# Performance work log

Measured on AMD Instinct MI355X. Metric: run time of the kernel, lower is better.

## Reference

```python
import jax, jax.numpy as jnp
import numpy as np

TWO_PI = 2.0 * np.pi
OMEGA = 1.0  # frequency scale from init


def setup_inputs() -> dict:
    key = jax.random.key(0)
    ks = jax.random.split(key, 10)
    B, G, D = 2, 32, 3
    C_IN, C, C_OUT, F, L = 4, 128, 2, 128, 4  # in/model/out channels, freqs, n_spectral_convs
    a = jax.random.normal(ks[0], (B, G, G, G, C_IN), dtype=jnp.float32)
    x = jax.random.uniform(ks[1], (B, G, G, G, D), dtype=jnp.float32)
    y = jax.random.uniform(ks[2], (B, G, G, G, D), dtype=jnp.float32)
    fc_in_w = jax.random.normal(ks[3], (C_IN, C), dtype=jnp.float32) / np.sqrt(C_IN)
    fc_in_b = jnp.zeros((C,), dtype=jnp.float32)
    freqs = jax.random.normal(ks[4], (L, F, D), dtype=jnp.float32)  # per-layer spatial frequencies
    w_real = jax.random.normal(ks[5], (L, C, C, F), dtype=jnp.float32) * 0.05
    w_imag = jax.random.normal(ks[6], (L, C, C, F), dtype=jnp.float32) * 0.05
    fc_out_w = jax.random.normal(ks[7], (C, C_OUT), dtype=jnp.float32) / np.sqrt(C)
    fc_out_b = jnp.zeros((C_OUT,), dtype=jnp.float32)
    return {"a": a, "x": x, "y": y, "fc_in_w": fc_in_w, "fc_in_b": fc_in_b,
            "freqs": freqs, "w_real": w_real, "w_imag": w_imag,
            "fc_out_w": fc_out_w, "fc_out_b": fc_out_b}


def _spectral_conv(hf, xin, xout, k, Wc):
    # hf: (B, N, C) real; xin/xout: (B, N, D); k: (F, D); Wc: (C, C, F) complex
    N = hf.shape[1]
    ang_in = TWO_PI * OMEGA * jnp.einsum('bnd,fd->bnf', xin, k)
    phi_in = jnp.exp(-1j * ang_in.astype(jnp.complex64))          # (B, N, F)
    H = jnp.einsum('bnc,bnf->bcf', hf.astype(jnp.complex64), phi_in) / N  # forward transform
    G = jnp.einsum('bcf,cof->bof', H, Wc)                          # per-frequency channel mixing
    ang_out = TWO_PI * OMEGA * jnp.einsum('bnd,fd->bnf', xout, k)
    phi_out = jnp.exp(1j * ang_out.astype(jnp.complex64))          # (B, N, F)
    return jnp.real(jnp.einsum('bof,bnf->bno', G, phi_out))       # inverse evaluation at xout


def reference(a, x, y, fc_in_w, fc_in_b, freqs, w_real, w_imag, fc_out_w, fc_out_b):
    B = a.shape[0]
    spatial = a.shape[1:4]
    hf = jnp.einsum('...i,io->...o', a, fc_in_w) + fc_in_b
    hf = hf.reshape(B, -1, hf.shape[-1])               # (B, N, C)
    xf = x.reshape(B, -1, x.shape[-1])                 # (B, N, D)
    yf = y.reshape(B, -1, y.shape[-1])
    L = freqs.shape[0]
    for l in range(L):
        Wc = (w_real[l] + 1j * w_imag[l]).astype(jnp.complex64)
        pts_out = xf if l < L - 1 else yf              # last conv queries at y
        hf = jax.nn.gelu(_spectral_conv(hf, xf, pts_out, freqs[l], Wc))
    u = jnp.einsum('bnc,co->bno', hf, fc_out_w) + fc_out_b
    return u.reshape(B, *spatial, fc_out_w.shape[-1])
```

## Files before the change

kernel.cpp:

```cpp
#include <hip/hip_runtime.h>
#include <math.h>

#define Bb 2
#define Nn 32768
#define Cc 128
#define Ff 128
#define LL 4
#define SKN 128
#define PS 16448

typedef __attribute__((ext_vector_type(8))) short short8;
typedef __attribute__((ext_vector_type(4))) float float4v;
typedef __attribute__((ext_vector_type(2))) unsigned int uint2v;
typedef unsigned short ushort_t;
typedef unsigned int uint_t;

union frag_cast { short8 s; uint_t u[4]; };
union vec8 { float4v v[2]; float s[8]; };

__device__ inline uint_t asu(float f) { union { float f; uint_t u; } x; x.f = f; return x.u; }
__device__ inline float asf(uint_t u) { union { uint_t u; float f; } x; x.u = u; return x.f; }
__device__ inline uint_t pack_hi(float v0, float v1) {
    return __builtin_amdgcn_perm(asu(v1), asu(v0), 0x07060302u);
}
__device__ inline float resid(float v) { return v - asf(asu(v) & 0xffff0000u); }

typedef __attribute__((address_space(1))) const uint_t guint;
typedef __attribute__((address_space(3))) uint_t luint;
__device__ inline void gload16(const uint_t* g, uint_t* l) {
    __builtin_amdgcn_global_load_lds((guint*)g, (luint*)l, 16, 0, 0);
}

__global__ __launch_bounds__(256) void prep_xt(const float* __restrict__ x,
                                               const float* __restrict__ y,
                                               float* __restrict__ xT,
                                               float* __restrict__ yT) {
    int i = blockIdx.x * 256 + threadIdx.x;
    int b = i >> 15, n = i & 32767;
    const float* xp = x + (size_t)i * 3;
    const float* yp = y + (size_t)i * 3;
    size_t base = ((size_t)(b * 3) << 15) + n;
    xT[base] = xp[0]; xT[base + (1 << 15)] = xp[1]; xT[base + (2 << 15)] = xp[2];
    yT[base] = yp[0]; yT[base + (1 << 15)] = yp[1]; yT[base + (2 << 15)] = yp[2];
}

__global__ __launch_bounds__(256) void in_proj(const float* __restrict__ a,
                                               const float* __restrict__ w,
                                               const float* __restrict__ bias,
                                               uint_t* __restrict__ hfTh,
                                               uint_t* __restrict__ hfTl) {
    int idx = blockIdx.x * 256 + threadIdx.x;
    int np = idx & 16383;
    int c = (idx >> 14) & 127;
    int b = idx >> 21;
    int n = np * 2;
    const float* ap = a + (((size_t)(b << 15)) + n) * 4;
    float s0 = bias[c], s1 = s0;
#pragma unroll
    for (int i = 0; i < 4; ++i) { s0 += ap[i] * w[i * Cc + c]; s1 += ap[4 + i] * w[i * Cc + c]; }
    hfTh[idx] = pack_hi(s0, s1);
    hfTl[idx] = pack_hi(resid(s0), resid(s1));
}

__global__ __launch_bounds__(256) void fwd_lds(const uint_t* __restrict__ hfTh,
                                               const uint_t* __restrict__ hfTl,
                                               const float* __restrict__ xT,
                                               const float* __restrict__ freqs,
                                               float* __restrict__ Spart) {
    __shared__ __align__(16) uint_t Ah_s[2][1024], Al_s[2][1024];

    const int sk = blockIdx.x;
    const int ct = blockIdx.y & 1, ft = blockIdx.y >> 1;
    const int b = blockIdx.z;
    const int tid = threadIdx.x, lane = tid & 63, wave = tid >> 6;
    const int h = wave & 1, wn = wave >> 1;
    const int fr = lane & 15, kg = lane >> 4;
    const int crow0 = b * 128 + ct * 64;

    float kx[2], ky[2], kz[2];
#pragma unroll
    for (int ni = 0; ni < 2; ++ni) {
        int f = ft * 64 + wn * 32 + ni * 16 + fr;
        kx[ni] = freqs[f * 3 + 0];
        ky[ni] = freqs[f * 3 + 1];
        kz[ni] = freqs[f * 3 + 2];
    }

    const float* xb = xT + ((size_t)(b * 3) << 15);

    const int srow = wave * 16 + (lane >> 2);
    const size_t gbase = ((size_t)(crow0 + srow) << 14) + (size_t)((lane & 3) * 4);
    const int npair0 = sk * 128;

    float4v acc[4][2];
#pragma unroll
    for (int mi = 0; mi < 4; ++mi)
#pragma unroll
        for (int ni = 0; ni < 2; ++ni) acc[mi][ni] = (float4v){0.f, 0.f, 0.f, 0.f};

    vec8 X0[2], X1[2], X2[2];
    gload16(hfTh + gbase + npair0, &Ah_s[0][wave * 256]);
    gload16(hfTl + gbase + npair0, &Al_s[0][wave * 256]);
    {
        const int nbase = sk * 256 + kg * 8;
        X0[0].v[0] = *(const float4v*)(xb + nbase);
        X0[0].v[1] = *(const float4v*)(xb + nbase + 4);
        X1[0].v[0] = *(const float4v*)(xb + (1 << 15) + nbase);
        X1[0].v[1] = *(const float4v*)(xb + (1 << 15) + nbase + 4);
        X2[0].v[0] = *(const float4v*)(xb + (2 << 15) + nbase);
        X2[0].v[1] = *(const float4v*)(xb + (2 << 15) + nbase + 4);
    }

#pragma unroll
    for (int kt = 0; kt < 8; ++kt) {
        const int cur = kt & 1, nxt = cur ^ 1;
        __syncthreads();
        if (kt < 7) {
            gload16(hfTh + gbase + npair0 + (kt + 1) * 16, &Ah_s[nxt][wave * 256]);
            gload16(hfTl + gbase + npair0 + (kt + 1) * 16, &Al_s[nxt][wave * 256]);
            const int nbase2 = sk * 256 + (kt + 1) * 32 + kg * 8;
            X0[nxt].v[0] = *(const float4v*)(xb + nbase2);
            X0[nxt].v[1] = *(const float4v*)(xb + nbase2 + 4);
            X1[nxt].v[0] = *(const float4v*)(xb + (1 << 15) + nbase2);
            X1[nxt].v[1] = *(const float4v*)(xb + (1 << 15) + nbase2 + 4);
            X2[nxt].v[0] = *(const float4v*)(xb + (2 << 15) + nbase2);
            X2[nxt].v[1] = *(const float4v*)(xb + (2 << 15) + nbase2 + 4);
        }
        float r[16], tv[16];
#pragma unroll
        for (int ni = 0; ni < 2; ++ni)
#pragma unroll
            for (int q = 0; q < 4; ++q) {
                float rv0 = X0[cur].s[2 * q] * kx[ni] + X1[cur].s[2 * q] * ky[ni] + X2[cur].s[2 * q] * kz[ni];
                float rv1 = X0[cur].s[2 * q + 1] * kx[ni] + X1[cur].s[2 * q + 1] * ky[ni] + X2[cur].s[2 * q + 1] * kz[ni];
                r[ni * 8 + 2 * q] = __builtin_amdgcn_fractf(rv0);
                r[ni * 8 + 2 * q + 1] = __builtin_amdgcn_fractf(rv1);
            }
        if (h) {
#pragma unroll
            for (int i = 0; i < 16; ++i) tv[i] = __builtin_amdgcn_sinf(r[i]);
        } else {
#pragma unroll
            for (int i = 0; i < 16; ++i) tv[i] = __builtin_amdgcn_cosf(r[i]);
        }
        frag_cast bh[2], bl[2];
#pragma unroll
        for (int ni = 0; ni < 2; ++ni)
#pragma unroll
            for (int q = 0; q < 4; ++q) {
                float v0 = tv[ni * 8 + 2 * q], v1 = tv[ni * 8 + 2 * q + 1];
                bh[ni].u[q] = pack_hi(v0, v1);
                bl[ni].u[q] = pack_hi(resid(v0), resid(v1));
            }
#pragma unroll
        for (int mi = 0; mi < 4; ++mi) {
            frag_cast ah, al;
            ah.s = *(const short8*)&Ah_s[cur][(mi * 16 + fr) * 16 + kg * 4];
            al.s = *(const short8*)&Al_s[cur][(mi * 16 + fr) * 16 + kg * 4];
#pragma unroll
            for (int ni = 0; ni < 2; ++ni) {
                acc[mi][ni] = __builtin_amdgcn_mfma_f32_16x16x32_bf16(ah.s, bh[ni].s, acc[mi][ni], 0, 0, 0);
                acc[mi][ni] = __builtin_amdgcn_mfma_f32_16x16x32_bf16(ah.s, bl[ni].s, acc[mi][ni], 0, 0, 0);
                acc[mi][ni] = __builtin_amdgcn_mfma_f32_16x16x32_bf16(al.s, bh[ni].s, acc[mi][ni], 0, 0, 0);
            }
        }
    }

    float* op = Spart + (size_t)((b * 2 + h) * SKN + sk) * PS;
#pragma unroll
    for (int mi = 0; mi < 4; ++mi)
#pragma unroll
        for (int ni = 0; ni < 2; ++ni)
#pragma unroll
            for (int r2 = 0; r2 < 4; ++r2) {
                int c = ct * 64 + mi * 16 + kg * 4 + r2;
                int f = ft * 64 + wn * 32 + ni * 16 + fr;
                op[c * 128 + f] = acc[mi][ni][r2];
            }
}

__global__ __launch_bounds__(256) void reduce_kernel(const float* __restrict__ Spart,
                                                     float* __restrict__ S) {
    __shared__ float red[4][64];
    const int chunk = blockIdx.x, bh = blockIdx.y;
    const int tid = threadIdx.x;
    const int cfl = tid & 63, q = tid >> 6;
    const float* p = Spart + (size_t)bh * SKN * PS + (size_t)(q * 32) * PS + chunk * 64 + cfl;
    float s = 0.0f;
#pragma unroll 8
    for (int k = 0; k < 32; ++k) s += p[(size_t)k * PS];
    red[q][cfl] = s;
    __syncthreads();
    if (tid < 64) {
        float t = red[0][tid] + red[1][tid] + red[2][tid] + red[3][tid];
        S[bh * 16384 + chunk * 64 + tid] = t;
    }
}

__global__ __launch_bounds__(256) void mix_kernel(const float* __restrict__ S,
                                                  const float* __restrict__ Wre,
                                                  const float* __restrict__ Wim,
                                                  uint_t* __restrict__ Gh,
                                                  uint_t* __restrict__ Gl) {
    __shared__ float Stile[4][128][16];
    const int ot = blockIdx.x;
    const int ft = blockIdx.y;
    const int tid = threadIdx.x;
    const int fl = tid & 15, ol = (tid >> 4) & 1, cg = tid >> 5;
    const int o = ot * 2 + ol, f0 = ft * 16;

    for (int i = tid; i < 8192; i += 256) {
        int bh = i >> 11, c = (i >> 4) & 127, ff = i & 15;
        Stile[bh][c][ff] = S[(size_t)bh * 16384 + c * 128 + f0 + ff];
    }
    __syncthreads();

    float g0 = 0.f, g1 = 0.f, g2 = 0.f, g3 = 0.f;
#pragma unroll 4
    for (int c = cg * 16; c < cg * 16 + 16; ++c) {
        float wr = Wre[((size_t)(c * 128 + o)) * 128 + f0 + fl];
        float wi = Wim[((size_t)(c * 128 + o)) * 128 + f0 + fl];
        float sc0 = Stile[0][c][fl], ss0 = Stile[1][c][fl];
        float sc1 = Stile[2][c][fl], ss1 = Stile[3][c][fl];
        g0 += sc0 * wr + ss0 * wi;  g1 += ss0 * wr - sc0 * wi;
        g2 += sc1 * wr + ss1 * wi;  g3 += ss1 * wr - sc1 * wi;
    }
    __syncthreads();
    float4v* rp = (float4v*)Stile;
    rp[cg * 32 + ol * 16 + fl] = (float4v){g0, g1, g2, g3};
    __syncthreads();
    if (tid < 32) {
        int tol = tid >> 4, tfl = tid & 15;
        float4v r = rp[tid];
#pragma unroll
        for (int j = 1; j < 8; ++j) r += rp[j * 32 + tid];
        const float invN = 1.0f / (float)Nn;
        float gre0 = r[0] * invN, gmi0 = r[1] * invN;
        float gre1 = r[2] * invN, gmi1 = r[3] * invN;
        int oo = ot * 2 + tol;
        Gh[(0 * 128 + oo) * 128 + f0 + tfl] = pack_hi(gre0, gmi0);
        Gl[(0 * 128 + oo) * 128 + f0 + tfl] = pack_hi(resid(gre0), resid(gmi0));
        Gh[(1 * 128 + oo) * 128 + f0 + tfl] = pack_hi(gre1, gmi1);
        Gl[(1 * 128 + oo) * 128 + f0 + tfl] = pack_hi(resid(gre1), resid(gmi1));
    }
}

__global__ __launch_bounds__(256, 2) void inv_reg(const uint_t* __restrict__ Gh,
                                                  const uint_t* __restrict__ Gl,
                                                  const float* __restrict__ ptsT,
                                                  const float* __restrict__ freqs,
                                                  uint_t* __restrict__ hfTh,
                                                  uint_t* __restrict__ hfTl) {
    __shared__ __align__(16) float kxs[128], kys[128], kzs[128];
    const int nt = blockIdx.x, b = blockIdx.y;
    const int tid = threadIdx.x, lane = tid & 63, wn = tid >> 6;
    const int fr = lane & 15, kg = lane >> 4;

    if (tid < 128) {
        kxs[tid] = freqs[tid * 3 + 0];
        kys[tid] = freqs[tid * 3 + 1];
        kzs[tid] = freqs[tid * 3 + 2];
    }
    __syncthreads();

    frag_cast bh[8][2], bl[8][2];
#pragma unroll
    for (int kt = 0; kt < 8; ++kt)
#pragma unroll
        for (int ni = 0; ni < 2; ++ni) {
            size_t gi = ((size_t)(b * 128 + wn * 32 + ni * 16 + fr)) * 128 + kt * 16 + kg * 4;
            bh[kt][ni].s = *(const short8*)(Gh + gi);
            bl[kt][ni].s = *(const short8*)(Gl + gi);
        }

    const float* pb = ptsT + ((size_t)(b * 3) << 15);
    const int stripe0 = nt * 128;

    for (int it = 0; it < 4; ++it) {
        const int n0 = stripe0 + it * 32;
        float px[2], py[2], pz[2];
#pragma unroll
        for (int mi = 0; mi < 2; ++mi) {
            int n = n0 + mi * 16 + fr;
            px[mi] = pb[n]; py[mi] = pb[(1 << 15) + n]; pz[mi] = pb[(2 << 15) + n];
        }
        float4v acc[2][2];
#pragma unroll
        for (int mi = 0; mi < 2; ++mi)
#pragma unroll
            for (int ni = 0; ni < 2; ++ni) acc[mi][ni] = (float4v){0.f, 0.f, 0.f, 0.f};

#pragma unroll
        for (int kt = 0; kt < 8; ++kt) {
            float4v kxv = *(const float4v*)&kxs[kt * 16 + kg * 4];
            float4v kyv = *(const float4v*)&kys[kt * 16 + kg * 4];
            float4v kzv = *(const float4v*)&kzs[kt * 16 + kg * 4];
#pragma unroll
            for (int mi = 0; mi < 2; ++mi) {
                frag_cast ah, al;
#pragma unroll
                for (int q = 0; q < 4; ++q) {
                    float rev = px[mi] * kxv[q] + py[mi] * kyv[q] + pz[mi] * kzv[q];
                    float rr = __builtin_amdgcn_fractf(rev);
                    float cv = __builtin_amdgcn_cosf(rr);
                    float sv = __builtin_amdgcn_sinf(rr);
                    ah.u[q] = pack_hi(cv, sv);
                    al.u[q] = pack_hi(resid(cv), resid(sv));
                }
#pragma unroll
                for (int ni = 0; ni < 2; ++ni) {
                    acc[mi][ni] = __builtin_amdgcn_mfma_f32_16x16x32_bf16(ah.s, bh[kt][ni].s, acc[mi][ni], 0, 0, 0);
                    acc[mi][ni] = __builtin_amdgcn_mfma_f32_16x16x32_bf16(ah.s, bl[kt][ni].s, acc[mi][ni], 0, 0, 0);
                    acc[mi][ni] = __builtin_amdgcn_mfma_f32_16x16x32_bf16(al.s, bh[kt][ni].s, acc[mi][ni], 0, 0, 0);
                }
            }
        }

#pragma unroll
        for (int mi = 0; mi < 2; ++mi)
#pragma unroll
            for (int ni = 0; ni < 2; ++ni) {
                float g[4];
#pragma unroll
                for (int r2 = 0; r2 < 4; ++r2) {
                    float v = acc[mi][ni][r2];
                    float u2 = 1.5957691216057308f * (v + 0.044715f * v * v * v);
                    float t = 1.0f - 2.0f / (1.0f + __expf(u2));
                    g[r2] = 0.5f * v * (1.0f + t);
                }
                int o = wn * 32 + ni * 16 + fr;
                int nb = n0 + mi * 16 + kg * 4;
                size_t di = ((size_t)(b * 128 + o) << 14) + (nb >> 1);
                uint2v hv = { pack_hi(g[0], g[1]), pack_hi(g[2], g[3]) };
                uint2v lv = { pack_hi(resid(g[0]), resid(g[1])), pack_hi(resid(g[2]), resid(g[3])) };
                *(uint2v*)(hfTh + di) = hv;
                *(uint2v*)(hfTl + di) = lv;
            }
    }
}

__global__ __launch_bounds__(256) void out_proj(const uint_t* __restrict__ hfTh,
                                                const uint_t* __restrict__ hfTl,
                                                const float* __restrict__ w,
                                                const float* __restrict__ bias,
                                                float* __restrict__ u) {
    int i = blockIdx.x * 256 + threadIdx.x;
    int b = i >> 14, np = i & 16383;
    const uint_t* hp = hfTh + ((size_t)(b * 128) << 14) + np;
    const uint_t* lp = hfTl + ((size_t)(b * 128) << 14) + np;
    float s0a = bias[0], s1a = bias[1], s0b = bias[0], s1b = bias[1];
#pragma unroll 4
    for (int c = 0; c < 128; ++c) {
        uint_t hv = hp[(size_t)c << 14], lv = lp[(size_t)c << 14];
        float v0 = asf(hv << 16) + asf(lv << 16);
        float v1 = asf(hv & 0xffff0000u) + asf(lv & 0xffff0000u);
        float w0 = w[c * 2 + 0], w1 = w[c * 2 + 1];
        s0a += v0 * w0; s1a += v0 * w1;
        s0b += v1 * w0; s1b += v1 * w1;
    }
    float4v o4 = {s0a, s1a, s0b, s1b};
    *(float4v*)(u + ((size_t)(b << 15) + np * 2) * 2) = o4;
}

extern "C" void kernel_launch(void* const* d_in, const int* in_sizes, int n_in,
                              void* d_out, int out_size, void* d_ws, size_t ws_size,
                              hipStream_t stream) {
    const float* a        = (const float*)d_in[0];
    const float* x        = (const float*)d_in[1];
    const float* y        = (const float*)d_in[2];
    const float* fc_in_w  = (const float*)d_in[3];
    const float* fc_in_b  = (const float*)d_in[4];
    const float* freqs    = (const float*)d_in[5];
    const float* w_real   = (const float*)d_in[6];
    const float* w_imag   = (const float*)d_in[7];
    const float* fc_out_w = (const float*)d_in[8];
    const float* fc_out_b = (const float*)d_in[9];
    float* out = (float*)d_out;

    uint_t* ws    = (uint_t*)d_ws;
    uint_t* hfTh  = ws;
    uint_t* hfTl  = hfTh + (size_t)Bb * Cc * Nn / 2;
    float*  Spart = (float*)(hfTl + (size_t)Bb * Cc * Nn / 2);
    float*  S     = Spart + (size_t)Bb * 2 * SKN * PS;
    uint_t* Gh    = (uint_t*)(S + (size_t)Bb * 2 * Cc * Ff);
    uint_t* Gl    = Gh + (size_t)Bb * Cc * Ff;
    float*  xT    = (float*)(Gl + (size_t)Bb * Cc * Ff);
    float*  yT    = xT + (size_t)Bb * 3 * Nn;

    prep_xt<<<(Bb * Nn) / 256, 256, 0, stream>>>(x, y, xT, yT);
    in_proj<<<(Bb * Cc * Nn / 2) / 256, 256, 0, stream>>>(a, fc_in_w, fc_in_b, hfTh, hfTl);

    for (int l = 0; l < LL; ++l) {
        const float* k   = freqs  + (size_t)l * Ff * 3;
        const float* Wre = w_real + (size_t)l * Cc * Cc * Ff;
        const float* Wim = w_imag + (size_t)l * Cc * Cc * Ff;
        const float* pT  = (l < LL - 1) ? xT : yT;

        fwd_lds<<<dim3(SKN, 4, Bb), 256, 0, stream>>>(hfTh, hfTl, xT, k, Spart);
        reduce_kernel<<<dim3(256, 4), 256, 0, stream>>>(Spart, S);
        mix_kernel<<<dim3(64, 8), 256, 0, stream>>>(S, Wre, Wim, Gh, Gl);
        inv_reg<<<dim3(256, Bb), 256, 0, stream>>>(Gh, Gl, pT, k, hfTh, hfTl);
    }

    out_proj<<<(Bb * Nn / 2) / 256, 256, 0, stream>>>(hfTh, hfTl, fc_out_w, fc_out_b, out);
}
```

Baseline: 402.3 us.

## Share inverse phase fragments via LDS and split output channels across blocks

The inverse kernel changes its work split. Each block now handles 32 points and half of the output channels, launched on a (1024,2,B) grid. Each wave computes the cos/sin fragments for only two of the eight frequency tiles and shares them through LDS, instead of every wave recomputing all of them. This cuts redundant transcendental work and register pressure, allowing 4 blocks per CU, but adds LDS barriers, doubles phase computation across the two channel-half blocks, and drops the per-block loop over four stripes. The forward kernel now stages the point coordinates into LDS with one async global-to-LDS load instead of per-iteration register loads, and also raises its occupancy hint to 4.

```diff
diff --git a/kernel.cpp b/kernel.cpp
--- a/kernel.cpp
+++ b/kernel.cpp
@@ -30,6 +30,8 @@
 __device__ inline void gload16(const uint_t* g, uint_t* l) {
     __builtin_amdgcn_global_load_lds((guint*)g, (luint*)l, 16, 0, 0);
 }
+
+#define LBAR() asm volatile("s_waitcnt lgkmcnt(0)\n\ts_barrier" ::: "memory")
 
 __global__ __launch_bounds__(256) void prep_xt(const float* __restrict__ x,
                                                const float* __restrict__ y,
@@ -62,12 +64,13 @@
     hfTl[idx] = pack_hi(resid(s0), resid(s1));
 }
 
-__global__ __launch_bounds__(256) void fwd_lds(const uint_t* __restrict__ hfTh,
-                                               const uint_t* __restrict__ hfTl,
-                                               const float* __restrict__ xT,
-                                               const float* __restrict__ freqs,
-                                               float* __restrict__ Spart) {
+__global__ __launch_bounds__(256, 4) void fwd_lds(const uint_t* __restrict__ hfTh,
+                                                  const uint_t* __restrict__ hfTl,
+                                                  const float* __restrict__ xT,
+                                                  const float* __restrict__ freqs,
+                                                  float* __restrict__ Spart) {
     __shared__ __align__(16) uint_t Ah_s[2][1024], Al_s[2][1024];
+    __shared__ __align__(16) float Xs[768];
 
     const int sk = blockIdx.x;
     const int ct = blockIdx.y & 1, ft = blockIdx.y >> 1;
@@ -98,18 +101,12 @@
 #pragma unroll
         for (int ni = 0; ni < 2; ++ni) acc[mi][ni] = (float4v){0.f, 0.f, 0.f, 0.f};
 
-    vec8 X0[2], X1[2], X2[2];
+    if (wave < 3) {
+        const uint_t* gx = (const uint_t*)xb + ((size_t)wave << 15) + sk * 256 + lane * 4;
+        gload16(gx, (uint_t*)&Xs[wave * 256]);
+    }
     gload16(hfTh + gbase + npair0, &Ah_s[0][wave * 256]);
     gload16(hfTl + gbase + npair0, &Al_s[0][wave * 256]);
-    {
-        const int nbase = sk * 256 + kg * 8;
-        X0[0].v[0] = *(const float4v*)(xb + nbase);
-        X0[0].v[1] = *(const float4v*)(xb + nbase + 4);
-        X1[0].v[0] = *(const float4v*)(xb + (1 << 15) + nbase);
-        X1[0].v[1] = *(const float4v*)(xb + (1 << 15) + nbase + 4);
-        X2[0].v[0] = *(const float4v*)(xb + (2 << 15) + nbase);
-        X2[0].v[1] = *(const float4v*)(xb + (2 << 15) + nbase + 4);
-    }
 
 #pragma unroll
     for (int kt = 0; kt < 8; ++kt) {
@@ -118,21 +115,21 @@
         if (kt < 7) {
             gload16(hfTh + gbase + npair0 + (kt + 1) * 16, &Ah_s[nxt][wave * 256]);
             gload16(hfTl + gbase + npair0 + (kt + 1) * 16, &Al_s[nxt][wave * 256]);
-            const int nbase2 = sk * 256 + (kt + 1) * 32 + kg * 8;
-            X0[nxt].v[0] = *(const float4v*)(xb + nbase2);
-            X0[nxt].v[1] = *(const float4v*)(xb + nbase2 + 4);
-            X1[nxt].v[0] = *(const float4v*)(xb + (1 << 15) + nbase2);
-            X1[nxt].v[1] = *(const float4v*)(xb + (1 << 15) + nbase2 + 4);
-            X2[nxt].v[0] = *(const float4v*)(xb + (2 << 15) + nbase2);
-            X2[nxt].v[1] = *(const float4v*)(xb + (2 << 15) + nbase2 + 4);
-        }
+        }
+        vec8 x0, x1, x2;
+        x0.v[0] = *(const float4v*)&Xs[0 * 256 + kt * 32 + kg * 8];
+        x0.v[1] = *(const float4v*)&Xs[0 * 256 + kt * 32 + kg * 8 + 4];
+        x1.v[0] = *(const float4v*)&Xs[1 * 256 + kt * 32 + kg * 8];
+        x1.v[1] = *(const float4v*)&Xs[1 * 256 + kt * 32 + kg * 8 + 4];
+        x2.v[0] = *(const float4v*)&Xs[2 * 256 + kt * 32 + kg * 8];
+        x2.v[1] = *(const float4v*)&Xs[2 * 256 + kt * 32 + kg * 8 + 4];
         float r[16], tv[16];
 #pragma unroll
         for (int ni = 0; ni < 2; ++ni)
 #pragma unroll
             for (int q = 0; q < 4; ++q) {
-                float rv0 = X0[cur].s[2 * q] * kx[ni] + X1[cur].s[2 * q] * ky[ni] + X2[cur].s[2 * q] * kz[ni];
-                float rv1 = X0[cur].s[2 * q + 1] * kx[ni] + X1[cur].s[2 * q + 1] * ky[ni] + X2[cur].s[2 * q + 1] * kz[ni];
+                float rv0 = x0.s[2 * q] * kx[ni] + x1.s[2 * q] * ky[ni] + x2.s[2 * q] * kz[ni];
+                float rv1 = x0.s[2 * q + 1] * kx[ni] + x1.s[2 * q + 1] * ky[ni] + x2.s[2 * q + 1] * kz[ni];
                 r[ni * 8 + 2 * q] = __builtin_amdgcn_fractf(rv0);
                 r[ni * 8 + 2 * q + 1] = __builtin_amdgcn_fractf(rv1);
             }
@@ -143,14 +140,14 @@
 #pragma unroll
             for (int i = 0; i < 16; ++i) tv[i] = __builtin_amdgcn_cosf(r[i]);
         }
-        frag_cast bh[2], bl[2];
+        frag_cast bhf[2], blf[2];
 #pragma unroll
         for (int ni = 0; ni < 2; ++ni)
 #pragma unroll
             for (int q = 0; q < 4; ++q) {
                 float v0 = tv[ni * 8 + 2 * q], v1 = tv[ni * 8 + 2 * q + 1];
-                bh[ni].u[q] = pack_hi(v0, v1);
-                bl[ni].u[q] = pack_hi(resid(v0), resid(v1));
+                bhf[ni].u[q] = pack_hi(v0, v1);
+                blf[ni].u[q] = pack_hi(resid(v0), resid(v1));
             }
 #pragma unroll
         for (int mi = 0; mi < 4; ++mi) {
@@ -159,9 +156,9 @@
             al.s = *(const short8*)&Al_s[cur][(mi * 16 + fr) * 16 + kg * 4];
 #pragma unroll
             for (int ni = 0; ni < 2; ++ni) {
-                acc[mi][ni] = __builtin_amdgcn_mfma_f32_16x16x32_bf16(ah.s, bh[ni].s, acc[mi][ni], 0, 0, 0);
-                acc[mi][ni] = __builtin_amdgcn_mfma_f32_16x16x32_bf16(ah.s, bl[ni].s, acc[mi][ni], 0, 0, 0);
-                acc[mi][ni] = __builtin_amdgcn_mfma_f32_16x16x32_bf16(al.s, bh[ni].s, acc[mi][ni], 0, 0, 0);
+                acc[mi][ni] = __builtin_amdgcn_mfma_f32_16x16x32_bf16(ah.s, bhf[ni].s, acc[mi][ni], 0, 0, 0);
+                acc[mi][ni] = __builtin_amdgcn_mfma_f32_16x16x32_bf16(ah.s, blf[ni].s, acc[mi][ni], 0, 0, 0);
+                acc[mi][ni] = __builtin_amdgcn_mfma_f32_16x16x32_bf16(al.s, bhf[ni].s, acc[mi][ni], 0, 0, 0);
             }
         }
     }
@@ -245,14 +242,16 @@
     }
 }
 
-__global__ __launch_bounds__(256, 2) void inv_reg(const uint_t* __restrict__ Gh,
+__global__ __launch_bounds__(256, 4) void inv_reg(const uint_t* __restrict__ Gh,
                                                   const uint_t* __restrict__ Gl,
                                                   const float* __restrict__ ptsT,
                                                   const float* __restrict__ freqs,
                                                   uint_t* __restrict__ hfTh,
                                                   uint_t* __restrict__ hfTl) {
     __shared__ __align__(16) float kxs[128], kys[128], kzs[128];
-    const int nt = blockIdx.x, b = blockIdx.y;
+    __shared__ __align__(16) uint_t Ah_s[2048];
+    __shared__ __align__(16) uint_t Al_s[2048];
+    const int nt = blockIdx.x, oh = blockIdx.y, b = blockIdx.z;
     const int tid = threadIdx.x, lane = tid & 63, wn = tid >> 6;
     const int fr = lane & 15, kg = lane >> 4;
 
@@ -261,81 +260,125 @@
         kys[tid] = freqs[tid * 3 + 1];
         kzs[tid] = freqs[tid * 3 + 2];
     }
+
+    frag_cast bh[8], bl[8];
+#pragma unroll
+    for (int kt = 0; kt < 8; ++kt) {
+        size_t gi = ((size_t)(b * 128 + oh * 64 + wn * 16 + fr)) * 128 + kt * 16 + kg * 4;
+        bh[kt].s = *(const short8*)(Gh + gi);
+        bl[kt].s = *(const short8*)(Gl + gi);
+    }
+
+    const float* pb = ptsT + ((size_t)(b * 3) << 15);
+    const int n0 = nt * 32;
+    float px[2], py[2], pz[2];
+#pragma unroll
+    for (int mi = 0; mi < 2; ++mi) {
+        int n = n0 + mi * 16 + fr;
+        px[mi] = pb[n]; py[mi] = pb[(1 << 15) + n]; pz[mi] = pb[(2 << 15) + n];
+    }
+
     __syncthreads();
 
-    frag_cast bh[8][2], bl[8][2];
-#pragma unroll
-    for (int kt = 0; kt < 8; ++kt)
-#pragma unroll
-        for (int ni = 0; ni < 2; ++ni) {
-            size_t gi = ((size_t)(b * 128 + wn * 32 + ni * 16 + fr)) * 128 + kt * 16 + kg * 4;
-            bh[kt][ni].s = *(const short8*)(Gh + gi);
-            bl[kt][ni].s = *(const short8*)(Gl + gi);
-        }
-
-    const float* pb = ptsT + ((size_t)(b * 3) << 15);
-    const int stripe0 = nt * 128;
-
-    for (int it = 0; it < 4; ++it) {
-        const int n0 = stripe0 + it * 32;
-        float px[2], py[2], pz[2];
-#pragma unroll
-        for (int mi = 0; mi < 2; ++mi) {
-            int n = n0 + mi * 16 + fr;
-            px[mi] = pb[n]; py[mi] = pb[(1 << 15) + n]; pz[mi] = pb[(2 << 15) + n];
-        }
-        float4v acc[2][2];
-#pragma unroll
-        for (int mi = 0; mi < 2; ++mi)
-#pragma unroll
-            for (int ni = 0; ni < 2; ++ni) acc[mi][ni] = (float4v){0.f, 0.f, 0.f, 0.f};
-
-#pragma unroll
-        for (int kt = 0; kt < 8; ++kt) {
-            float4v kxv = *(const float4v*)&kxs[kt * 16 + kg * 4];
-            float4v kyv = *(const float4v*)&kys[kt * 16 + kg * 4];
-            float4v kzv = *(const float4v*)&kzs[kt * 16 + kg * 4];
-#pragma unroll
-            for (int mi = 0; mi < 2; ++mi) {
-                frag_cast ah, al;
-#pragma unroll
-                for (int q = 0; q < 4; ++q) {
-                    float rev = px[mi] * kxv[q] + py[mi] * kyv[q] + pz[mi] * kzv[q];
-                    float rr = __builtin_amdgcn_fractf(rev);
-                    float cv = __builtin_amdgcn_cosf(rr);
-                    float sv = __builtin_amdgcn_sinf(rr);
-                    ah.u[q] = pack_hi(cv, sv);
-                    al.u[q] = pack_hi(resid(cv), resid(sv));
-                }
-#pragma unroll
-                for (int ni = 0; ni < 2; ++ni) {
-                    acc[mi][ni] = __builtin_amdgcn_mfma_f32_16x16x32_bf16(ah.s, bh[kt][ni].s, acc[mi][ni], 0, 0, 0);
-                    acc[mi][ni] = __builtin_amdgcn_mfma_f32_16x16x32_bf16(ah.s, bl[kt][ni].s, acc[mi][ni], 0, 0, 0);
-                    acc[mi][ni] = __builtin_amdgcn_mfma_f32_16x16x32_bf16(al.s, bh[kt][ni].s, acc[mi][ni], 0, 0, 0);
-                }
-            }
-        }
-
-#pragma unroll
-        for (int mi = 0; mi < 2; ++mi)
-#pragma unroll
-            for (int ni = 0; ni < 2; ++ni) {
-                float g[4];
-#pragma unroll
-                for (int r2 = 0; r2 < 4; ++r2) {
-                    float v = acc[mi][ni][r2];
-                    float u2 = 1.5957691216057308f * (v + 0.044715f * v * v * v);
-                    float t = 1.0f - 2.0f / (1.0f + __expf(u2));
-                    g[r2] = 0.5f * v * (1.0f + t);
-                }
-                int o = wn * 32 + ni * 16 + fr;
-                int nb = n0 + mi * 16 + kg * 4;
-                size_t di = ((size_t)(b * 128 + o) << 14) + (nb >> 1);
-                uint2v hv = { pack_hi(g[0], g[1]), pack_hi(g[2], g[3]) };
-                uint2v lv = { pack_hi(resid(g[0]), resid(g[1])), pack_hi(resid(g[2]), resid(g[3])) };
-                *(uint2v*)(hfTh + di) = hv;
-                *(uint2v*)(hfTl + di) = lv;
-            }
+    float4v acc[2];
+#pragma unroll
+    for (int mi = 0; mi < 2; ++mi) acc[mi] = (float4v){0.f, 0.f, 0.f, 0.f};
+
+#pragma unroll
+    for (int kk = 0; kk < 2; ++kk) {
+        const int kt = wn * 2 + kk;
+        float4v kxv = *(const float4v*)&kxs[kt * 16 + kg * 4];
+        float4v kyv = *(const float4v*)&kys[kt * 16 + kg * 4];
+        float4v kzv = *(const float4v*)&kzs[kt * 16 + kg * 4];
+        frag_cast ah, al;
+#pragma unroll
+        for (int q = 0; q < 4; ++q) {
+            float rev = px[0] * kxv[q] + py[0] * kyv[q] + pz[0] * kzv[q];
+            float rr = __builtin_amdgcn_fractf(rev);
+            float cv = __builtin_amdgcn_cosf(rr);
+            float sv = __builtin_amdgcn_sinf(rr);
+            ah.u[q] = pack_hi(cv, sv);
+            al.u[q] = pack_hi(resid(cv), resid(sv));
+        }
+        *(short8*)&Ah_s[(kt * 64 + lane) * 4] = ah.s;
+        *(short8*)&Al_s[(kt * 64 + lane) * 4] = al.s;
+    }
+    LBAR();
+
+#pragma unroll
+    for (int kt = 0; kt < 8; ++kt) {
+        frag_cast ah, al;
+        ah.s = *(const short8*)&Ah_s[(kt * 64 + lane) * 4];
+        al.s = *(const short8*)&Al_s[(kt * 64 + lane) * 4];
+        acc[0] = __builtin_amdgcn_mfma_f32_16x16x32_bf16(ah.s, bh[kt].s, acc[0], 0, 0, 0);
+        acc[0] = __builtin_amdgcn_mfma_f32_16x16x32_bf16(ah.s, bl[kt].s, acc[0], 0, 0, 0);
+        acc[0] = __builtin_amdgcn_mfma_f32_16x16x32_bf16(al.s, bh[kt].s, acc[0], 0, 0, 0);
+    }
+    LBAR();
+
+#pragma unroll
+    for (int kk = 0; kk < 2; ++kk) {
+        const int kt = wn * 2 + kk;
+        float4v kxv = *(const float4v*)&kxs[kt * 16 + kg * 4];
+        float4v kyv = *(const float4v*)&kys[kt * 16 + kg * 4];
+        float4v kzv = *(const float4v*)&kzs[kt * 16 + kg * 4];
+        frag_cast ah, al;
+#pragma unroll
+        for (int q = 0; q < 4; ++q) {
+            float rev = px[1] * kxv[q] + py[1] * kyv[q] + pz[1] * kzv[q];
+            float rr = __builtin_amdgcn_fractf(rev);
+            float cv = __builtin_amdgcn_cosf(rr);
+            float sv = __builtin_amdgcn_sinf(rr);
+            ah.u[q] = pack_hi(cv, sv);
+            al.u[q] = pack_hi(resid(cv), resid(sv));
+        }
+        *(short8*)&Ah_s[(kt * 64 + lane) * 4] = ah.s;
+        *(short8*)&Al_s[(kt * 64 + lane) * 4] = al.s;
+    }
+    {
+        float g[4];
+#pragma unroll
+        for (int r2 = 0; r2 < 4; ++r2) {
+            float v = acc[0][r2];
+            float u2 = 1.5957691216057308f * (v + 0.044715f * v * v * v);
+            float t = 1.0f - 2.0f / (1.0f + __expf(u2));
+            g[r2] = 0.5f * v * (1.0f + t);
+        }
+        int o = oh * 64 + wn * 16 + fr;
+        int nb = n0 + 0 * 16 + kg * 4;
+        size_t di = ((size_t)(b * 128 + o) << 14) + (nb >> 1);
+        uint2v hv = { pack_hi(g[0], g[1]), pack_hi(g[2], g[3]) };
+        uint2v lv = { pack_hi(resid(g[0]), resid(g[1])), pack_hi(resid(g[2]), resid(g[3])) };
+        *(uint2v*)(hfTh + di) = hv;
+        *(uint2v*)(hfTl + di) = lv;
+    }
+    LBAR();
+
+#pragma unroll
+    for (int kt = 0; kt < 8; ++kt) {
+        frag_cast ah, al;
+        ah.s = *(const short8*)&Ah_s[(kt * 64 + lane) * 4];
+        al.s = *(const short8*)&Al_s[(kt * 64 + lane) * 4];
+        acc[1] = __builtin_amdgcn_mfma_f32_16x16x32_bf16(ah.s, bh[kt].s, acc[1], 0, 0, 0);
+        acc[1] = __builtin_amdgcn_mfma_f32_16x16x32_bf16(ah.s, bl[kt].s, acc[1], 0, 0, 0);
+        acc[1] = __builtin_amdgcn_mfma_f32_16x16x32_bf16(al.s, bh[kt].s, acc[1], 0, 0, 0);
+    }
+    {
+        float g[4];
+#pragma unroll
+        for (int r2 = 0; r2 < 4; ++r2) {
+            float v = acc[1][r2];
+            float u2 = 1.5957691216057308f * (v + 0.044715f * v * v * v);
+            float t = 1.0f - 2.0f / (1.0f + __expf(u2));
+            g[r2] = 0.5f * v * (1.0f + t);
+        }
+        int o = oh * 64 + wn * 16 + fr;
+        int nb = n0 + 1 * 16 + kg * 4;
+        size_t di = ((size_t)(b * 128 + o) << 14) + (nb >> 1);
+        uint2v hv = { pack_hi(g[0], g[1]), pack_hi(g[2], g[3]) };
+        uint2v lv = { pack_hi(resid(g[0]), resid(g[1])), pack_hi(resid(g[2]), resid(g[3])) };
+        *(uint2v*)(hfTh + di) = hv;
+        *(uint2v*)(hfTl + di) = lv;
     }
 }
 
@@ -399,7 +442,7 @@
         fwd_lds<<<dim3(SKN, 4, Bb), 256, 0, stream>>>(hfTh, hfTl, xT, k, Spart);
         reduce_kernel<<<dim3(256, 4), 256, 0, stream>>>(Spart, S);
         mix_kernel<<<dim3(64, 8), 256, 0, stream>>>(S, Wre, Wim, Gh, Gl);
-        inv_reg<<<dim3(256, Bb), 256, 0, stream>>>(Gh, Gl, pT, k, hfTh, hfTl);
+        inv_reg<<<dim3(1024, 2, Bb), 256, 0, stream>>>(Gh, Gl, pT, k, hfTh, hfTl);
     }
 
     out_proj<<<(Bb * Nn / 2) / 256, 256, 0, stream>>>(hfTh, hfTl, fc_out_w, fc_out_b, out);
```

Result: no change. 407.6 us (+1.3%).

## Share inverse-transform phase fragments across warps via double-buffered LDS

Applied to the files above, without the earlier changes.

In the inverse kernel, every warp previously recomputed the cos/sin phase fragments for all 8 frequency tiles of each 32-point chunk. Now each warp computes only its 2 frequency tiles per 16-point slab, writes them to a double-buffered LDS array, and all warps read the full set, which cuts redundant sin/cos work by about four times. The next slab's phases are computed before the MFMAs of the current one and stored after them, overlapping trig with matrix work. The three split-bf16 products now go into separate accumulators to break the MFMA dependency chain. The cost is a barrier per slab and extra LDS traffic and footprint, which may lower occupancy.

```diff
diff --git a/kernel.cpp b/kernel.cpp
--- a/kernel.cpp
+++ b/kernel.cpp
@@ -30,6 +30,8 @@
 __device__ inline void gload16(const uint_t* g, uint_t* l) {
     __builtin_amdgcn_global_load_lds((guint*)g, (luint*)l, 16, 0, 0);
 }
+
+#define LBAR() asm volatile("s_waitcnt lgkmcnt(0)\n\ts_barrier" ::: "memory")
 
 __global__ __launch_bounds__(256) void prep_xt(const float* __restrict__ x,
                                                const float* __restrict__ y,
@@ -143,14 +145,14 @@
 #pragma unroll
             for (int i = 0; i < 16; ++i) tv[i] = __builtin_amdgcn_cosf(r[i]);
         }
-        frag_cast bh[2], bl[2];
+        frag_cast bhf[2], blf[2];
 #pragma unroll
         for (int ni = 0; ni < 2; ++ni)
 #pragma unroll
             for (int q = 0; q < 4; ++q) {
                 float v0 = tv[ni * 8 + 2 * q], v1 = tv[ni * 8 + 2 * q + 1];
-                bh[ni].u[q] = pack_hi(v0, v1);
-                bl[ni].u[q] = pack_hi(resid(v0), resid(v1));
+                bhf[ni].u[q] = pack_hi(v0, v1);
+                blf[ni].u[q] = pack_hi(resid(v0), resid(v1));
             }
 #pragma unroll
         for (int mi = 0; mi < 4; ++mi) {
@@ -159,9 +161,9 @@
             al.s = *(const short8*)&Al_s[cur][(mi * 16 + fr) * 16 + kg * 4];
 #pragma unroll
             for (int ni = 0; ni < 2; ++ni) {
-                acc[mi][ni] = __builtin_amdgcn_mfma_f32_16x16x32_bf16(ah.s, bh[ni].s, acc[mi][ni], 0, 0, 0);
-                acc[mi][ni] = __builtin_amdgcn_mfma_f32_16x16x32_bf16(ah.s, bl[ni].s, acc[mi][ni], 0, 0, 0);
-                acc[mi][ni] = __builtin_amdgcn_mfma_f32_16x16x32_bf16(al.s, bh[ni].s, acc[mi][ni], 0, 0, 0);
+                acc[mi][ni] = __builtin_amdgcn_mfma_f32_16x16x32_bf16(ah.s, bhf[ni].s, acc[mi][ni], 0, 0, 0);
+                acc[mi][ni] = __builtin_amdgcn_mfma_f32_16x16x32_bf16(ah.s, blf[ni].s, acc[mi][ni], 0, 0, 0);
+                acc[mi][ni] = __builtin_amdgcn_mfma_f32_16x16x32_bf16(al.s, bhf[ni].s, acc[mi][ni], 0, 0, 0);
             }
         }
     }
@@ -252,6 +254,8 @@
                                                   uint_t* __restrict__ hfTh,
                                                   uint_t* __restrict__ hfTl) {
     __shared__ __align__(16) float kxs[128], kys[128], kzs[128];
+    __shared__ __align__(16) uint_t Ah_s[2][2048];
+    __shared__ __align__(16) uint_t Al_s[2][2048];
     const int nt = blockIdx.x, b = blockIdx.y;
     const int tid = threadIdx.x, lane = tid & 63, wn = tid >> 6;
     const int fr = lane & 15, kg = lane >> 4;
@@ -261,7 +265,6 @@
         kys[tid] = freqs[tid * 3 + 1];
         kzs[tid] = freqs[tid * 3 + 2];
     }
-    __syncthreads();
 
     frag_cast bh[8][2], bl[8][2];
 #pragma unroll
@@ -274,68 +277,111 @@
         }
 
     const float* pb = ptsT + ((size_t)(b * 3) << 15);
-    const int stripe0 = nt * 128;
-
-    for (int it = 0; it < 4; ++it) {
-        const int n0 = stripe0 + it * 32;
-        float px[2], py[2], pz[2];
-#pragma unroll
-        for (int mi = 0; mi < 2; ++mi) {
-            int n = n0 + mi * 16 + fr;
-            px[mi] = pb[n]; py[mi] = pb[(1 << 15) + n]; pz[mi] = pb[(2 << 15) + n];
-        }
-        float4v acc[2][2];
-#pragma unroll
-        for (int mi = 0; mi < 2; ++mi)
-#pragma unroll
-            for (int ni = 0; ni < 2; ++ni) acc[mi][ni] = (float4v){0.f, 0.f, 0.f, 0.f};
-
-#pragma unroll
-        for (int kt = 0; kt < 8; ++kt) {
-            float4v kxv = *(const float4v*)&kxs[kt * 16 + kg * 4];
-            float4v kyv = *(const float4v*)&kys[kt * 16 + kg * 4];
-            float4v kzv = *(const float4v*)&kzs[kt * 16 + kg * 4];
-#pragma unroll
-            for (int mi = 0; mi < 2; ++mi) {
-                frag_cast ah, al;
+    const int n0 = nt * 128;
+
+    float px[8], py[8], pz[8];
+#pragma unroll
+    for (int p = 0; p < 8; ++p) {
+        int n = n0 + p * 16 + fr;
+        px[p] = pb[n]; py[p] = pb[(1 << 15) + n]; pz[p] = pb[(2 << 15) + n];
+    }
+
+    __syncthreads();
+
+#pragma unroll
+    for (int kk = 0; kk < 2; ++kk) {
+        const int kt = wn * 2 + kk;
+        float4v kxv = *(const float4v*)&kxs[kt * 16 + kg * 4];
+        float4v kyv = *(const float4v*)&kys[kt * 16 + kg * 4];
+        float4v kzv = *(const float4v*)&kzs[kt * 16 + kg * 4];
+        frag_cast ah, al;
+#pragma unroll
+        for (int q = 0; q < 4; ++q) {
+            float rev = px[0] * kxv[q] + py[0] * kyv[q] + pz[0] * kzv[q];
+            float rr = __builtin_amdgcn_fractf(rev);
+            float cv = __builtin_amdgcn_cosf(rr);
+            float sv = __builtin_amdgcn_sinf(rr);
+            ah.u[q] = pack_hi(cv, sv);
+            al.u[q] = pack_hi(resid(cv), resid(sv));
+        }
+        *(short8*)&Ah_s[0][(kt * 64 + lane) * 4] = ah.s;
+        *(short8*)&Al_s[0][(kt * 64 + lane) * 4] = al.s;
+    }
+    LBAR();
+
+#pragma unroll
+    for (int p = 0; p < 8; ++p) {
+        const int cur = p & 1, nxt = cur ^ 1;
+
+        frag_cast tah[2], tal[2];
+        if (p < 7) {
+#pragma unroll
+            for (int kk = 0; kk < 2; ++kk) {
+                const int kt = wn * 2 + kk;
+                float4v kxv = *(const float4v*)&kxs[kt * 16 + kg * 4];
+                float4v kyv = *(const float4v*)&kys[kt * 16 + kg * 4];
+                float4v kzv = *(const float4v*)&kzs[kt * 16 + kg * 4];
 #pragma unroll
                 for (int q = 0; q < 4; ++q) {
-                    float rev = px[mi] * kxv[q] + py[mi] * kyv[q] + pz[mi] * kzv[q];
+                    float rev = px[p + 1] * kxv[q] + py[p + 1] * kyv[q] + pz[p + 1] * kzv[q];
                     float rr = __builtin_amdgcn_fractf(rev);
                     float cv = __builtin_amdgcn_cosf(rr);
                     float sv = __builtin_amdgcn_sinf(rr);
-                    ah.u[q] = pack_hi(cv, sv);
-                    al.u[q] = pack_hi(resid(cv), resid(sv));
+                    tah[kk].u[q] = pack_hi(cv, sv);
+                    tal[kk].u[q] = pack_hi(resid(cv), resid(sv));
                 }
-#pragma unroll
-                for (int ni = 0; ni < 2; ++ni) {
-                    acc[mi][ni] = __builtin_amdgcn_mfma_f32_16x16x32_bf16(ah.s, bh[kt][ni].s, acc[mi][ni], 0, 0, 0);
-                    acc[mi][ni] = __builtin_amdgcn_mfma_f32_16x16x32_bf16(ah.s, bl[kt][ni].s, acc[mi][ni], 0, 0, 0);
-                    acc[mi][ni] = __builtin_amdgcn_mfma_f32_16x16x32_bf16(al.s, bh[kt][ni].s, acc[mi][ni], 0, 0, 0);
-                }
-            }
-        }
-
-#pragma unroll
-        for (int mi = 0; mi < 2; ++mi)
+            }
+        }
+
+        float4v ahh[2], ahl[2], alh[2];
+#pragma unroll
+        for (int ni = 0; ni < 2; ++ni) {
+            ahh[ni] = (float4v){0.f, 0.f, 0.f, 0.f};
+            ahl[ni] = (float4v){0.f, 0.f, 0.f, 0.f};
+            alh[ni] = (float4v){0.f, 0.f, 0.f, 0.f};
+        }
+#pragma unroll
+        for (int kt = 0; kt < 8; ++kt) {
+            frag_cast ah, al;
+            ah.s = *(const short8*)&Ah_s[cur][(kt * 64 + lane) * 4];
+            al.s = *(const short8*)&Al_s[cur][(kt * 64 + lane) * 4];
 #pragma unroll
             for (int ni = 0; ni < 2; ++ni) {
-                float g[4];
-#pragma unroll
-                for (int r2 = 0; r2 < 4; ++r2) {
-                    float v = acc[mi][ni][r2];
-                    float u2 = 1.5957691216057308f * (v + 0.044715f * v * v * v);
-                    float t = 1.0f - 2.0f / (1.0f + __expf(u2));
-                    g[r2] = 0.5f * v * (1.0f + t);
-                }
-                int o = wn * 32 + ni * 16 + fr;
-                int nb = n0 + mi * 16 + kg * 4;
-                size_t di = ((size_t)(b * 128 + o) << 14) + (nb >> 1);
-                uint2v hv = { pack_hi(g[0], g[1]), pack_hi(g[2], g[3]) };
-                uint2v lv = { pack_hi(resid(g[0]), resid(g[1])), pack_hi(resid(g[2]), resid(g[3])) };
-                *(uint2v*)(hfTh + di) = hv;
-                *(uint2v*)(hfTl + di) = lv;
-            }
+                ahh[ni] = __builtin_amdgcn_mfma_f32_16x16x32_bf16(ah.s, bh[kt][ni].s, ahh[ni], 0, 0, 0);
+                ahl[ni] = __builtin_amdgcn_mfma_f32_16x16x32_bf16(ah.s, bl[kt][ni].s, ahl[ni], 0, 0, 0);
+                alh[ni] = __builtin_amdgcn_mfma_f32_16x16x32_bf16(al.s, bh[kt][ni].s, alh[ni], 0, 0, 0);
+            }
+        }
+
+        if (p < 7) {
+#pragma unroll
+            for (int kk = 0; kk < 2; ++kk) {
+                const int kt = wn * 2 + kk;
+                *(short8*)&Ah_s[nxt][(kt * 64 + lane) * 4] = tah[kk].s;
+                *(short8*)&Al_s[nxt][(kt * 64 + lane) * 4] = tal[kk].s;
+            }
+        }
+
+#pragma unroll
+        for (int ni = 0; ni < 2; ++ni) {
+            float g[4];
+#pragma unroll
+            for (int r2 = 0; r2 < 4; ++r2) {
+                float v = ahh[ni][r2] + (ahl[ni][r2] + alh[ni][r2]);
+                float u2 = 1.5957691216057308f * (v + 0.044715f * v * v * v);
+                float t = 1.0f - 2.0f / (1.0f + __expf(u2));
+                g[r2] = 0.5f * v * (1.0f + t);
+            }
+            int o = wn * 32 + ni * 16 + fr;
+            int nb = n0 + p * 16 + kg * 4;
+            size_t di = ((size_t)(b * 128 + o) << 14) + (nb >> 1);
+            uint2v hv = { pack_hi(g[0], g[1]), pack_hi(g[2], g[3]) };
+            uint2v lv = { pack_hi(resid(g[0]), resid(g[1])), pack_hi(resid(g[2]), resid(g[3])) };
+            *(uint2v*)(hfTh + di) = hv;
+            *(uint2v*)(hfTl + di) = lv;
+        }
+
+        LBAR();
     }
 }
 
```

New measurement: 378.2 us. 1.06x faster.
